# Performance work log

Hardware: AMD Instinct MI355X
Metric: run time of the kernel (lower is better)

## Reference

```python
import jax, jax.numpy as jnp
import numpy as np
from jax import lax

E, H, V, S, T, B = 128, 254, 32000, 50, 50, 64


def setup_inputs() -> dict:
    key = jax.random.key(0)
    ks = jax.random.split(key, 14)
    sc = 0.05
    n = lambda k, shape: jax.random.normal(k, shape, dtype=jnp.float32) * sc
    return {
        "src": jax.random.randint(ks[0], (S, B), 0, V),
        "trg": jax.random.randint(ks[1], (T, B), 0, V),
        "emb_enc": n(ks[2], (V, E)),
        "W_ih_e": n(ks[3], (3 * H, E)),
        "W_hh_e": n(ks[4], (3 * H, H)),
        "b_ih_e": n(ks[5], (3 * H,)),
        "b_hh_e": n(ks[6], (3 * H,)),
        "emb_dec": n(ks[7], (V, E)),
        "W_ih_d": n(ks[8], (3 * H, E + H)),
        "W_hh_d": n(ks[9], (3 * H, H)),
        "b_ih_d": n(ks[10], (3 * H,)),
        "b_hh_d": n(ks[11], (3 * H,)),
        "W_out": n(ks[12], (V, E + 2 * H)),
        "b_out": n(ks[13], (V,)),
    }


def _gru_cell(x, h, W_ih, W_hh, b_ih, b_hh):
    # PyTorch GRU cell: gates ordered [r, z, n]
    gi = x @ W_ih.T + b_ih            # [B, 3H]
    gh = h @ W_hh.T + b_hh            # [B, 3H]
    i_r, i_z, i_n = jnp.split(gi, 3, axis=-1)
    h_r, h_z, h_n = jnp.split(gh, 3, axis=-1)
    r = jax.nn.sigmoid(i_r + h_r)
    z = jax.nn.sigmoid(i_z + h_z)
    n = jnp.tanh(i_n + r * h_n)
    return (1.0 - z) * n + z * h


def reference(src, trg, emb_enc, W_ih_e, W_hh_e, b_ih_e, b_hh_e,
              emb_dec, W_ih_d, W_hh_d, b_ih_d, b_hh_d, W_out, b_out):
    dt = emb_enc.dtype
    # --- Encoder: GRU over src (dropout = identity in eval) ---
    enc_emb = emb_enc[src]                       # [S, B, E]
    h0 = jnp.zeros((B, H), dtype=dt)

    def enc_step(h, x):
        h2 = _gru_cell(x, h, W_ih_e, W_hh_e, b_ih_e, b_hh_e)
        return h2, None

    context, _ = lax.scan(enc_step, h0, enc_emb)  # [B, H]

    # --- Decoder: teacher forcing (ratio=1.0) => scan over trg[:-1] ---
    dec_emb = emb_dec[trg[:-1]]                  # [T-1, B, E]

    def dec_step(h, e):
        xc = jnp.concatenate([e, context], axis=-1)          # [B, E+H]
        h2 = _gru_cell(xc, h, W_ih_d, W_hh_d, b_ih_d, b_hh_d)
        feat = jnp.concatenate([h2, context, e], axis=-1)    # [B, E+2H]
        pred = feat @ W_out.T + b_out                        # [B, V]
        return h2, pred

    _, preds = lax.scan(dec_step, context, dec_emb)  # [T-1, B, V]
    outputs = jnp.concatenate(
        [jnp.zeros((1, B, V), dtype=preds.dtype), preds], axis=0)  # [T, B, V]
    return outputs
```

## Files before the change

### kernel.cpp

```cpp
#include <hip/hip_runtime.h>
#include <cstdint>
#include <cstddef>

typedef unsigned short u16;
typedef unsigned int u32;
typedef __attribute__((ext_vector_type(8))) short bf16x8;
typedef __attribute__((ext_vector_type(4))) float f32x4;

#define AS1 __attribute__((address_space(1)))
#define AS3 __attribute__((address_space(3)))

__device__ __forceinline__ float bf2f(u16 u){ u32 x = ((u32)u)<<16; float f; __builtin_memcpy(&f,&x,4); return f; }
__device__ __forceinline__ u16 f2bf(float f){ u32 x; __builtin_memcpy(&x,&f,4); u32 r=(x+0x7FFFu+((x>>16)&1u))>>16; return (u16)r; }

__device__ __forceinline__ float fast_sig(float x){
  return __fdividef(1.f, 1.f + __expf(-x));
}
__device__ __forceinline__ float fast_tanh(float x){
  float e = __expf(2.f*x);
  return 1.f - __fdividef(2.f, e + 1.f);
}


__global__ void zero_bytes(uint4* p, size_t n16){
  size_t i = (size_t)blockIdx.x*blockDim.x + threadIdx.x;
  size_t st = (size_t)gridDim.x*blockDim.x;
  uint4 z; z.x=0u; z.y=0u; z.z=0u; z.w=0u;
  for (; i<n16; i+=st) p[i]=z;
}

__global__ void pad_convert_g(const float* __restrict__ src, int src_ld, int c0, int vcols,
                              u16* __restrict__ dst, int dcols){
  int i = blockIdx.x*256 + threadIdx.x;
  int tot = 768*dcols;
  if (i >= tot) return;
  int p = i/dcols, c = i - p*dcols;
  int wv = p/96, rem = p - wv*96, sec = rem>>5, u = rem&31;
  int j = wv*32 + u;
  float v = 0.f;
  if (j < 254 && c < vcols) v = src[(size_t)(sec*254 + j)*src_ld + c0 + c];
  dst[i] = f2bf(v);
}

__global__ void pad_bias_comb(const float* __restrict__ ih, const float* __restrict__ hh,
                              float* __restrict__ dst){
  int p = blockIdx.x*256 + threadIdx.x;
  if (p >= 768) return;
  int wv = p/96, rem = p - wv*96, sec = rem>>5, u = rem&31;
  int j = wv*32 + u;
  float v = 0.f;
  if (j < 254){ v = ih[sec*254 + j]; if (sec < 2) v += hh[sec*254 + j]; }
  dst[p] = v;
}

__global__ void pad_bias_g(const float* __restrict__ src, float* __restrict__ dst){
  int p = blockIdx.x*256 + threadIdx.x;
  if (p >= 768) return;
  int wv = p/96, rem = p - wv*96, sec = rem>>5, u = rem&31;
  int j = wv*32 + u;
  dst[p] = (j<254) ? src[sec*254 + j] : 0.f;
}

__global__ void gather_enc(const int* __restrict__ idx, const float* __restrict__ emb, u16* __restrict__ dst){
  int i = blockIdx.x*256 + threadIdx.x;
  int r = i>>7, k = i&127;
  dst[i] = f2bf(emb[(size_t)idx[r]*128 + k]);
}

__global__ void gather_dec(const int* __restrict__ idx, const float* __restrict__ emb,
                           u16* __restrict__ dst, u16* __restrict__ feat){
  int i = blockIdx.x*256 + threadIdx.x;
  int r = i>>7, k = i&127;
  u16 v = 0;
  if (r < 3136) v = f2bf(emb[(size_t)idx[r]*128 + k]);
  dst[i] = v;
  if (r < 3136) feat[(size_t)r*640 + 508 + k] = v;
}


__global__ __launch_bounds__(256) void gemm_bt(
  const u16* __restrict__ A, int lda,
  const u16* __restrict__ B, int ldb,
  float* __restrict__ C, long long ldc,
  const float* __restrict__ bias,
  int K, int Mtiles, int Mstore)
{
  __shared__ __align__(16) u16 Abuf[2][128*64];
  __shared__ __align__(16) u16 Bbuf[2][128*64];
  const int t = threadIdx.x;
  const int w = t>>6, l = t&63;
  const int wm = w>>1, wn = w&1;
  const int mt = blockIdx.x % Mtiles, nt = blockIdx.x / Mtiles;
  const int m0 = mt<<7, n0 = nt<<7;

  const int lr = l>>3, lg = l&7;

  auto stage = [&](const u16* __restrict__ G, int ld, int base0, int k0, u16* Lbuf){
    #pragma unroll
    for (int i=0;i<4;++i){
      const int rbase = i*32 + w*8;
      const int r = rbase + lr;
      const int gsw = lg ^ (r&7);
      __builtin_amdgcn_global_load_lds(
        (const AS1 void*)(G + (size_t)(base0+r)*ld + k0 + gsw*8),
        (AS3 void*)(Lbuf + rbase*64), 16, 0, 0);
    }
  };

  f32x4 acc[4][4] = {};
  const int ksteps = K>>6;

  stage(A, lda, m0, 0, Abuf[0]);
  stage(B, ldb, n0, 0, Bbuf[0]);
  asm volatile("s_waitcnt vmcnt(0)" ::: "memory");
  __syncthreads();

  for (int ks=0; ks<ksteps; ++ks){
    const int cb = ks&1;
    if (ks+1 < ksteps){
      stage(A, lda, m0, (ks+1)<<6, Abuf[cb^1]);
      stage(B, ldb, n0, (ks+1)<<6, Bbuf[cb^1]);
    }
    const u16* Al = Abuf[cb];
    const u16* Bl = Bbuf[cb];
    #pragma unroll
    for (int kk=0;kk<2;++kk){
      const int ko = kk*32 + (l>>4)*8;
      bf16x8 af[4], bfr[4];
      #pragma unroll
      for (int m=0;m<4;++m){
        const int row = wm*64+m*16+(l&15);
        af[m] = *(const bf16x8*)&Al[row*64 + (ko ^ ((row&7)<<3))];
      }
      #pragma unroll
      for (int n=0;n<4;++n){
        const int row = wn*64+n*16+(l&15);
        bfr[n] = *(const bf16x8*)&Bl[row*64 + (ko ^ ((row&7)<<3))];
      }
      #pragma unroll
      for (int m=0;m<4;++m)
        #pragma unroll
        for (int n=0;n<4;++n)
          acc[m][n] = __builtin_amdgcn_mfma_f32_16x16x32_bf16(af[m], bfr[n], acc[m][n], 0,0,0);
    }
    asm volatile("s_waitcnt vmcnt(0)" ::: "memory");
    __syncthreads();
  }

  float bv[4];
  #pragma unroll
  for (int n=0;n<4;++n) bv[n] = bias[n0 + wn*64 + n*16 + (l&15)];
  #pragma unroll
  for (int m=0;m<4;++m){
    const int rb = m0 + wm*64 + m*16 + (l>>4)*4;
    #pragma unroll
    for (int n=0;n<4;++n){
      const int col = n0 + wn*64 + n*16 + (l&15);
      #pragma unroll
      for (int r=0;r<4;++r){
        const int rr = rb + r;
        if (rr < Mstore) C[(size_t)rr*ldc + col] = acc[m][n][r] + bv[n];
      }
    }
  }
}


__global__ __launch_bounds__(512,1) void fused_scan_gemm(
  const u16* Whhe, const u16* Whhd, const u16* Wihdc,
  const float* bhhe, const float* bhhd,
  const float* enc_gi, const float* dec_gi,
  u16* feat, u16* wout_b, const float* W_out,
  float* Cg, const float* b_out, u32* ctr)
{
  __shared__ __align__(16) char smem[139776];
  const int t = threadIdx.x;
  const int w = t>>6, l = t&63;

  if (blockIdx.x < 4){
    const int g = blockIdx.x;
    const int la = l&15, q = l>>4;
    const int brow0 = g*16;

    u16*   hb   = (u16*)smem;
    float* gib  = (float*)(smem + 16896);
    u16*   ctxb = (u16*)(smem + 115200);

    bf16x8 Bf[48];

    auto loadW = [&](const u16* __restrict__ W){
      #pragma unroll
      for (int nt=0; nt<6; ++nt)
        #pragma unroll
        for (int kk=0; kk<8; ++kk)
          Bf[nt*8+kk] = *(const bf16x8*)&W[(size_t)(w*96 + nt*16 + la)*256 + kk*32 + q*8];
    };

    auto stage = [&](const float* __restrict__ gsrc, int step, float* dstL){
      const float* src = gsrc + (size_t)(step*64 + brow0)*768;
      #pragma unroll
      for (int i=0;i<6;++i){
        const int base = i*2048 + w*256;
        __builtin_amdgcn_global_load_lds((const AS1 void*)(src + base + l*4),
                                         (AS3 void*)(dstL + base), 16, 0, 0);
      }
    };

    auto mm = [&](const u16* hsrc, f32x4* acc){
      #pragma unroll
      for (int kk=0; kk<8; ++kk){
        bf16x8 a = *(const bf16x8*)&hsrc[la*264 + kk*32 + q*8];
        #pragma unroll
        for (int nt=0; nt<6; ++nt)
          acc[nt] = __builtin_amdgcn_mfma_f32_16x16x32_bf16(a, Bf[nt*8+kk], acc[nt], 0,0,0);
      }
    };

    for (int i=t; i<2*16*264; i+=512) hb[i] = 0;
    stage(enc_gi, 0, gib);
    loadW(Whhe);
    float bn[2];
    #pragma unroll
    for (int tl=0; tl<2; ++tl) bn[tl] = bhhe[w*96 + tl*16 + la + 64];
    asm volatile("s_waitcnt vmcnt(0)" ::: "memory");
    __syncthreads();

    #pragma unroll 1
    for (int s=0; s<50; ++s){
      const int cur = s&1;
      if (s < 49) stage(enc_gi, s+1, gib + (cur^1)*12288);
      f32x4 acc[6] = {};
      mm(hb + cur*4224, acc);
      #pragma unroll
      for (int tl=0; tl<2; ++tl){
        const int pb = w*96 + tl*16 + la;
        const int j  = w*32 + tl*16 + la;
        #pragma unroll
        for (int r=0;r<4;++r){
          const int b = q*4 + r;
          const float gir = gib[cur*12288 + b*768 + pb];
          const float giz = gib[cur*12288 + b*768 + pb + 32];
          const float gin = gib[cur*12288 + b*768 + pb + 64];
          const float ho = bf2f(hb[cur*4224 + b*264 + j]);
          const float rg = fast_sig(gir + acc[tl][r]);
          const float zg = fast_sig(giz + acc[2+tl][r]);
          const float ng = fast_tanh(gin + rg*(acc[4+tl][r] + bn[tl]));
          hb[(cur^1)*4224 + b*264 + j] = f2bf((1.f-zg)*ng + zg*ho);
        }
      }
      asm volatile("s_waitcnt vmcnt(0)" ::: "memory");
      __syncthreads();
    }

    stage(dec_gi, 0, gib);

    loadW(Wihdc);
    {
      f32x4 acc[6] = {};
      mm(hb, acc);
      #pragma unroll
      for (int nt=0; nt<6; ++nt)
        #pragma unroll
        for (int r=0;r<4;++r)
          ctxb[(q*4+r)*768 + w*96 + nt*16 + la] = f2bf(acc[nt][r]);
    }

    #pragma unroll 1
    for (int i=t; i<49*4096; i+=512){
      const int tt = i>>12, rem = i&4095, b = rem>>8, c = rem&255;
      if (c < 254) feat[(size_t)(tt*64 + brow0 + b)*640 + 254 + c] = hb[b*264 + c];
    }

    loadW(Whhd);
    #pragma unroll
    for (int tl=0; tl<2; ++tl) bn[tl] = bhhd[w*96 + tl*16 + la + 64];
    asm volatile("s_waitcnt vmcnt(0)" ::: "memory");
    __syncthreads();

    #pragma unroll 1
    for (int tt=0; tt<49; ++tt){
      const int cur = tt&1;
      if (tt < 48) stage(dec_gi, tt+1, gib + (cur^1)*12288);
      f32x4 acc[6] = {};
      mm(hb + cur*4224, acc);
      #pragma unroll
      for (int tl=0; tl<2; ++tl){
        const int pb = w*96 + tl*16 + la;
        const int j  = w*32 + tl*16 + la;
        #pragma unroll
        for (int r=0;r<4;++r){
          const int b = q*4 + r;
          const float gir = gib[cur*12288 + b*768 + pb]      + bf2f(ctxb[b*768 + pb]);
          const float giz = gib[cur*12288 + b*768 + pb + 32] + bf2f(ctxb[b*768 + pb + 32]);
          const float gin = gib[cur*12288 + b*768 + pb + 64] + bf2f(ctxb[b*768 + pb + 64]);
          const float ho = bf2f(hb[cur*4224 + b*264 + j]);
          const float rg = fast_sig(gir + acc[tl][r]);
          const float zg = fast_sig(giz + acc[2+tl][r]);
          const float ng = fast_tanh(gin + rg*(acc[4+tl][r] + bn[tl]));
          const float h2 = (1.f-zg)*ng + zg*ho;
          const u16 hbv = f2bf(h2);
          hb[(cur^1)*4224 + b*264 + j] = hbv;
          if (j < 254) feat[(size_t)(tt*64 + brow0 + b)*640 + j] = hbv;
        }
      }
      asm volatile("s_waitcnt vmcnt(0)" ::: "memory");
      __syncthreads();
      if (t==0)
        __hip_atomic_store(&ctr[g*32], (u32)(tt+1), __ATOMIC_RELEASE, __HIP_MEMORY_SCOPE_AGENT);
    }
    return;
  }

  const int bg = blockIdx.x - 4;
  const int wm = w>>2, wn = w&3;
  const int la = l&15, q = l>>4;
  const int lr = l>>3, lg = l&7;

  u16* AL = (u16*)smem;
  u16* BL = (u16*)(smem + 32768);

  if (bg < 125){
    const int n0c = bg<<8;
    #pragma unroll 1
    for (int i=t; i<256*80; i+=512){
      const int r = i/80, c8 = (i - r*80)<<3;
      u16 o[8];
      #pragma unroll
      for (int jj=0;jj<8;++jj){
        const int c = c8 + jj;
        o[jj] = (c < 636) ? f2bf(W_out[(size_t)(n0c+r)*636 + c]) : (u16)0;
      }
      *(uint4*)&wout_b[(size_t)(n0c+r)*640 + c8] = *(uint4*)o;
    }
    __syncthreads();
    if (t==0)
      __hip_atomic_store(&ctr[128 + bg*32], 1u, __ATOMIC_RELEASE, __HIP_MEMORY_SCOPE_AGENT);
  }

  #pragma unroll 1
  for (int tau = bg; tau < 3125; tau += 248){
    const int mt = tau/125, nt = tau - mt*125;
    const int m0 = mt<<7, n0 = nt<<8;
    const u32 need = (u32)((2*mt+2 < 49) ? (2*mt+2) : 49);

    if (w==0){
      int cnt = 0;
      while (true){
        u32 v  = (l<4) ? __hip_atomic_load(&ctr[l*32], __ATOMIC_RELAXED, __HIP_MEMORY_SCOPE_AGENT) : 0xFFFFFFFFu;
        u32 wf = (l==4) ? __hip_atomic_load(&ctr[128 + nt*32], __ATOMIC_RELAXED, __HIP_MEMORY_SCOPE_AGENT) : 1u;
        if (__all((int)((v >= need) && (wf != 0u)))) break;
        __builtin_amdgcn_s_sleep(16);
        if (++cnt > (1<<22)) break;
      }
      (void)__hip_atomic_load(&ctr[0], __ATOMIC_ACQUIRE, __HIP_MEMORY_SCOPE_AGENT);
    }
    __syncthreads();

    auto stageA = [&](int k0, int buf){
      #pragma unroll
      for (int i=0;i<2;++i){
        const int rbase = i*64 + w*8;
        const int r = rbase + lr;
        __builtin_amdgcn_global_load_lds(
          (const AS1 void*)(feat + (size_t)(m0+r)*640 + k0 + ((lg^lr)<<3)),
          (AS3 void*)(AL + buf*8192 + rbase*64), 16, 0, 0);
      }
    };
    auto stageB = [&](int k0, int buf){
      #pragma unroll
      for (int i=0;i<4;++i){
        const int rbase = i*64 + w*8;
        const int r = rbase + lr;
        __builtin_amdgcn_global_load_lds(
          (const AS1 void*)(wout_b + (size_t)(n0+r)*640 + k0 + ((lg^lr)<<3)),
          (AS3 void*)(BL + buf*16384 + rbase*64), 16, 0, 0);
      }
    };

    f32x4 acc[4][4] = {};
    stageA(0,0); stageB(0,0);
    asm volatile("s_waitcnt vmcnt(0)" ::: "memory");
    __syncthreads();

    #pragma unroll 1
    for (int ks=0; ks<10; ++ks){
      const int cb = ks&1;
      if (ks < 9){ stageA((ks+1)<<6, cb^1); stageB((ks+1)<<6, cb^1); }
      const u16* Alp = AL + cb*8192;
      const u16* Blp = BL + cb*16384;
      #pragma unroll
      for (int kk=0;kk<2;++kk){
        const int ko = kk*32 + q*8;
        bf16x8 af[4], bfr[4];
        #pragma unroll
        for (int m=0;m<4;++m){
          const int row = wm*64 + m*16 + la;
          af[m] = *(const bf16x8*)&Alp[row*64 + (ko ^ ((row&7)<<3))];
        }
        #pragma unroll
        for (int n=0;n<4;++n){
          const int row = wn*64 + n*16 + la;
          bfr[n] = *(const bf16x8*)&Blp[row*64 + (ko ^ ((row&7)<<3))];
        }
        #pragma unroll
        for (int m=0;m<4;++m)
          #pragma unroll
          for (int n=0;n<4;++n)
            acc[m][n] = __builtin_amdgcn_mfma_f32_16x16x32_bf16(af[m], bfr[n], acc[m][n], 0,0,0);
      }
      asm volatile("s_waitcnt vmcnt(0)" ::: "memory");
      __syncthreads();
    }

    float bv[4];
    #pragma unroll
    for (int n=0;n<4;++n) bv[n] = b_out[n0 + wn*64 + n*16 + la];
    #pragma unroll
    for (int m=0;m<4;++m){
      const int rb = m0 + wm*64 + m*16 + q*4;
      #pragma unroll
      for (int n=0;n<4;++n){
        const int col = n0 + wn*64 + n*16 + la;
        #pragma unroll
        for (int r=0;r<4;++r){
          const int rr = rb + r;
          if (rr < 3136)
            __builtin_nontemporal_store(acc[m][n][r] + bv[n], &Cg[(size_t)rr*32000 + col]);
        }
      }
    }
  }
}


extern "C" void kernel_launch(void* const* d_in, const int* in_sizes, int n_in,
                              void* d_out, int out_size, void* d_ws, size_t ws_size,
                              hipStream_t stream) {
  const int*   src     = (const int*)d_in[0];
  const int*   trg     = (const int*)d_in[1];
  const float* emb_enc = (const float*)d_in[2];
  const float* W_ih_e  = (const float*)d_in[3];
  const float* W_hh_e  = (const float*)d_in[4];
  const float* b_ih_e  = (const float*)d_in[5];
  const float* b_hh_e  = (const float*)d_in[6];
  const float* emb_dec = (const float*)d_in[7];
  const float* W_ih_d  = (const float*)d_in[8];
  const float* W_hh_d  = (const float*)d_in[9];
  const float* b_ih_d  = (const float*)d_in[10];
  const float* b_hh_d  = (const float*)d_in[11];
  const float* W_out   = (const float*)d_in[12];
  const float* b_out   = (const float*)d_in[13];
  float* out = (float*)d_out;

  char* basep = (char*)d_ws;
  size_t off = 0;
  auto take = [&](size_t b)->char*{ char* p = basep + off; off = (off + b + 255) & ~(size_t)255; return p; };
  u16* feat    = (u16*)take(4096000);
  u32* ctr     = (u32*)take(16640);
  u16* wout_b  = (u16*)take(40960000);
  u16* wihe_b  = (u16*)take(196608);
  u16* wihde_b = (u16*)take(196608);
  u16* wihdc_b = (u16*)take(393216);
  u16* whhe_b  = (u16*)take(393216);
  u16* whhd_b  = (u16*)take(393216);
  u16* encx_b  = (u16*)take(819200);
  u16* dece_b  = (u16*)take(819200);
  float* enc_gi = (float*)take(9830400);
  float* dec_gi = (float*)take(9830400);
  float* bihe_p = (float*)take(3072);
  float* bihd_p = (float*)take(3072);
  float* bhhe_p = (float*)take(3072);
  float* bhhd_p = (float*)take(3072);
  (void)in_sizes; (void)n_in; (void)out_size; (void)ws_size;

  zero_bytes<<<512, 256, 0, stream>>>((uint4*)feat, (size_t)((4096000+16640)/16));
  zero_bytes<<<2000, 256, 0, stream>>>((uint4*)out, (size_t)(8192000/16));

  pad_convert_g<<<384, 256, 0, stream>>>(W_ih_e, 128,   0, 128, wihe_b, 128);
  pad_convert_g<<<384, 256, 0, stream>>>(W_ih_d, 382,   0, 128, wihde_b, 128);
  pad_convert_g<<<768, 256, 0, stream>>>(W_ih_d, 382, 128, 254, wihdc_b, 256);
  pad_convert_g<<<768, 256, 0, stream>>>(W_hh_e, 254,   0, 254, whhe_b, 256);
  pad_convert_g<<<768, 256, 0, stream>>>(W_hh_d, 254,   0, 254, whhd_b, 256);

  pad_bias_comb<<<3, 256, 0, stream>>>(b_ih_e, b_hh_e, bihe_p);
  pad_bias_comb<<<3, 256, 0, stream>>>(b_ih_d, b_hh_d, bihd_p);
  pad_bias_g<<<3, 256, 0, stream>>>(b_hh_e, bhhe_p);
  pad_bias_g<<<3, 256, 0, stream>>>(b_hh_d, bhhd_p);

  gather_enc<<<1600, 256, 0, stream>>>(src, emb_enc, encx_b);
  gather_dec<<<1600, 256, 0, stream>>>(trg, emb_dec, dece_b, feat);

  gemm_bt<<<25*6, 256, 0, stream>>>(encx_b, 128, wihe_b, 128, enc_gi, (long long)768, bihe_p, 128, 25, 3200);
  gemm_bt<<<25*6, 256, 0, stream>>>(dece_b, 128, wihde_b, 128, dec_gi, (long long)768, bihd_p, 128, 25, 3200);

  fused_scan_gemm<<<252, 512, 0, stream>>>(whhe_b, whhd_b, wihdc_b, bhhe_p, bhhd_p,
                                           enc_gi, dec_gi, feat, wout_b, W_out,
                                           out + (size_t)64*32000, b_out, ctr);
}
```

Baseline: 560.1 us.

## Replace release/acquire flag sync with relaxed device-scope stores and packed counters

The producer-consumer handshake between the recurrent blocks and the output-GEMM blocks now uses relaxed agent-scope atomic stores for feature rows, converted weights and counters, instead of plain stores followed by a release store and an acquire load. Counters are packed contiguously rather than padded to 128 bytes, and waiting blocks back off with a staggered sleep count. The large zeroing of the feature buffer is dropped so that only the counter region is cleared. This cuts fence and cache-writeback overhead and initialization traffic, but correctness now depends on relaxed stores plus s_waitcnt being visible across CUs, and packed counters may share cache lines. Skipping the zeroing may also leave padding columns of the feature buffer uninitialized.

```diff
diff --git a/kernel.cpp b/kernel.cpp
--- a/kernel.cpp
+++ b/kernel.cpp
@@ -19,6 +19,13 @@
 __device__ __forceinline__ float fast_tanh(float x){
   float e = __expf(2.f*x);
   return 1.f - __fdividef(2.f, e + 1.f);
+}
+
+__device__ __forceinline__ void dev_store_u16(u16* p, u16 v){
+  __hip_atomic_store(p, v, __ATOMIC_RELAXED, __HIP_MEMORY_SCOPE_AGENT);
+}
+__device__ __forceinline__ void dev_store_u32(u32* p, u32 v){
+  __hip_atomic_store(p, v, __ATOMIC_RELAXED, __HIP_MEMORY_SCOPE_AGENT);
 }
 
 
@@ -268,7 +275,7 @@
     #pragma unroll 1
     for (int i=t; i<49*4096; i+=512){
       const int tt = i>>12, rem = i&4095, b = rem>>8, c = rem&255;
-      if (c < 254) feat[(size_t)(tt*64 + brow0 + b)*640 + 254 + c] = hb[b*264 + c];
+      if (c < 254) dev_store_u16(&feat[(size_t)(tt*64 + brow0 + b)*640 + 254 + c], hb[b*264 + c]);
     }
 
     loadW(Whhd);
@@ -300,13 +307,12 @@
           const float h2 = (1.f-zg)*ng + zg*ho;
           const u16 hbv = f2bf(h2);
           hb[(cur^1)*4224 + b*264 + j] = hbv;
-          if (j < 254) feat[(size_t)(tt*64 + brow0 + b)*640 + j] = hbv;
+          if (j < 254) dev_store_u16(&feat[(size_t)(tt*64 + brow0 + b)*640 + j], hbv);
         }
       }
       asm volatile("s_waitcnt vmcnt(0)" ::: "memory");
       __syncthreads();
-      if (t==0)
-        __hip_atomic_store(&ctr[g*32], (u32)(tt+1), __ATOMIC_RELEASE, __HIP_MEMORY_SCOPE_AGENT);
+      if (t==0) dev_store_u32(&ctr[g], (u32)(tt+1));
     }
     return;
   }
@@ -330,13 +336,17 @@
         const int c = c8 + jj;
         o[jj] = (c < 636) ? f2bf(W_out[(size_t)(n0c+r)*636 + c]) : (u16)0;
       }
-      *(uint4*)&wout_b[(size_t)(n0c+r)*640 + c8] = *(uint4*)o;
-    }
+      u32* dst = (u32*)&wout_b[(size_t)(n0c+r)*640 + c8];
+      const u32* sv = (const u32*)o;
+      #pragma unroll
+      for (int jj=0;jj<4;++jj) dev_store_u32(&dst[jj], sv[jj]);
+    }
+    asm volatile("s_waitcnt vmcnt(0)" ::: "memory");
     __syncthreads();
-    if (t==0)
-      __hip_atomic_store(&ctr[128 + bg*32], 1u, __ATOMIC_RELEASE, __HIP_MEMORY_SCOPE_AGENT);
+    if (t==0) dev_store_u32(&ctr[32 + bg], 1u);
   }
 
+  const int nsleep = 1 + (bg&3);
   #pragma unroll 1
   for (int tau = bg; tau < 3125; tau += 248){
     const int mt = tau/125, nt = tau - mt*125;
@@ -346,13 +356,12 @@
     if (w==0){
       int cnt = 0;
       while (true){
-        u32 v  = (l<4) ? __hip_atomic_load(&ctr[l*32], __ATOMIC_RELAXED, __HIP_MEMORY_SCOPE_AGENT) : 0xFFFFFFFFu;
-        u32 wf = (l==4) ? __hip_atomic_load(&ctr[128 + nt*32], __ATOMIC_RELAXED, __HIP_MEMORY_SCOPE_AGENT) : 1u;
+        u32 v  = (l<4) ? __hip_atomic_load(&ctr[l], __ATOMIC_RELAXED, __HIP_MEMORY_SCOPE_AGENT) : 0xFFFFFFFFu;
+        u32 wf = (l==4) ? __hip_atomic_load(&ctr[32 + nt], __ATOMIC_RELAXED, __HIP_MEMORY_SCOPE_AGENT) : 1u;
         if (__all((int)((v >= need) && (wf != 0u)))) break;
-        __builtin_amdgcn_s_sleep(16);
+        for (int z=0; z<nsleep; ++z) __builtin_amdgcn_s_sleep(16);
         if (++cnt > (1<<22)) break;
       }
-      (void)__hip_atomic_load(&ctr[0], __ATOMIC_ACQUIRE, __HIP_MEMORY_SCOPE_AGENT);
     }
     __syncthreads();
 
@@ -456,7 +465,7 @@
   size_t off = 0;
   auto take = [&](size_t b)->char*{ char* p = basep + off; off = (off + b + 255) & ~(size_t)255; return p; };
   u16* feat    = (u16*)take(4096000);
-  u32* ctr     = (u32*)take(16640);
+  u32* ctr     = (u32*)take(4096);
   u16* wout_b  = (u16*)take(40960000);
   u16* wihe_b  = (u16*)take(196608);
   u16* wihde_b = (u16*)take(196608);
@@ -473,7 +482,7 @@
   float* bhhd_p = (float*)take(3072);
   (void)in_sizes; (void)n_in; (void)out_size; (void)ws_size;
 
-  zero_bytes<<<512, 256, 0, stream>>>((uint4*)feat, (size_t)((4096000+16640)/16));
+  zero_bytes<<<1, 256, 0, stream>>>((uint4*)ctr, (size_t)(4096/16));
   zero_bytes<<<2000, 256, 0, stream>>>((uint4*)out, (size_t)(8192000/16));
 
   pad_convert_g<<<384, 256, 0, stream>>>(W_ih_e, 128,   0, 128, wihe_b, 128);
```

Result: no change. 560.1 us (-0.0%).
